# Kernel tuning notes

Hardware: AMD Instinct MI355X
Metric: run time of the kernel (lower is better)

The kernel has to match this reference:

```python
import jax, jax.numpy as jnp
import numpy as np

N = 50000      # nodes
F = 128        # in_features
OUT = 128      # out_features
E = 600000     # edges per adjacency (avg degree 12)
J = 2
BN_EPS = 1e-5


def setup_inputs() -> dict:
    key = jax.random.key(0)
    ks = jax.random.split(key, 10)
    x = jax.random.normal(ks[0], (N, F), dtype=jnp.float32)
    rows0 = jax.random.randint(ks[1], (E,), 0, N, dtype=jnp.int32)
    cols0 = jax.random.randint(ks[2], (E,), 0, N, dtype=jnp.int32)
    vals0 = jax.random.uniform(ks[3], (E,), dtype=jnp.float32)
    rows1 = jax.random.randint(ks[4], (E,), 0, N, dtype=jnp.int32)
    cols1 = jax.random.randint(ks[5], (E,), 0, N, dtype=jnp.int32)
    vals1 = jax.random.uniform(ks[6], (E,), dtype=jnp.float32)
    # Linear(J*F, OUT) params, torch default init U(-1/sqrt(fan_in), 1/sqrt(fan_in))
    lim = 1.0 / np.sqrt(J * F)
    W_fc = jax.random.uniform(ks[7], (OUT, J * F), dtype=jnp.float32, minval=-lim, maxval=lim)
    b_fc = jax.random.uniform(ks[8], (OUT,), dtype=jnp.float32, minval=-lim, maxval=lim)
    gamma = jnp.ones((OUT,), dtype=jnp.float32)
    beta = jnp.zeros((OUT,), dtype=jnp.float32)
    return {"x": x, "rows0": rows0, "cols0": cols0, "vals0": vals0,
            "rows1": rows1, "cols1": cols1, "vals1": vals1,
            "W_fc": W_fc, "b_fc": b_fc, "gamma": gamma, "beta": beta}


def _spmm(rows, cols, vals, x):
    # sparse [N,N] @ dense [N,F]: gather source features, weight, scatter-add to rows
    msgs = vals[:, None] * x[cols]                      # [E, F]
    return jax.ops.segment_sum(msgs, rows, num_segments=x.shape[0])  # [N, F]


def reference(x, rows0, cols0, vals0, rows1, cols1, vals1, W_fc, b_fc, gamma, beta):
    h = jnp.concatenate([_spmm(rows0, cols0, vals0, x),
                         _spmm(rows1, cols1, vals1, x)], axis=1)  # [N, J*F]
    y = h @ W_fc.T + b_fc                                         # [N, OUT]
    # BatchNorm1d (training mode: batch stats, biased variance)
    mean = jnp.mean(y, axis=0)
    var = jnp.mean((y - mean) ** 2, axis=0)
    return (y - mean) * jax.lax.rsqrt(var + BN_EPS) * gamma + beta
```

## Files before the change

### kernel.cpp

```cpp
#include <hip/hip_runtime.h>

#define N_NODES 50000
#define F_IN 128
#define OUT_F 128
#define JF 256
#define EDGES 600000
#define BN_EPS 1e-5f
#define MAXDEG 48
#define NPART 8
#define PART_ROWS 6250
#define BKCAP 163840
#define LCAP 256
#define EB_PER_SIDE 586
#define EDGE_B (2*EB_PER_SIDE)
#define CONVX_B 6250
#define CONVW_B 32
#define BUILDA_B (EDGE_B + CONVX_B + CONVW_B)
#define SCATB_B 1024
#define ROWS_PB 16
#define GATH_B 3125
#define GEMM_ROWS 32
#define GEMM_B 1563
#define HPAD 50048
#define NCOPY 16

typedef __attribute__((ext_vector_type(8))) short short8;
typedef __attribute__((ext_vector_type(4))) float floatx4;
typedef __attribute__((ext_vector_type(4))) unsigned short ushortx4;

static __device__ __forceinline__ unsigned short f2bf(float f) {
    unsigned int x = __float_as_uint(f);
    unsigned int r = (x + 0x7fffu + ((x >> 16) & 1u)) >> 16;
    return (unsigned short)r;
}
static __device__ __forceinline__ float bflo(unsigned int p) { return __uint_as_float(p << 16); }
static __device__ __forceinline__ float bfhi(unsigned int p) { return __uint_as_float(p & 0xffff0000u); }

__global__ __launch_bounds__(256) void build_a(
    const int* __restrict__ rows0, const int* __restrict__ cols0, const float* __restrict__ vals0,
    const int* __restrict__ rows1, const int* __restrict__ cols1, const float* __restrict__ vals1,
    uint2* __restrict__ buckets, int* __restrict__ gcur,
    const floatx4* __restrict__ x4, ushortx4* __restrict__ xb4,
    const float* __restrict__ W, uint2* __restrict__ Wb2)
{
    int bid = blockIdx.x;
    int tid = threadIdx.x;
    if (bid < EDGE_B) {
        __shared__ int   lcnt_[NPART];
        __shared__ int   lbase[NPART];
        __shared__ uint2 lbuf[NPART][LCAP];

        if (tid < NPART) lcnt_[tid] = 0;
        __syncthreads();

        int side = bid >= EB_PER_SIDE;
        int b = side ? bid - EB_PER_SIDE : bid;
        const int*   rows = side ? rows1 : rows0;
        const int*   cols = side ? cols1 : cols0;
        const float* vals = side ? vals1 : vals0;

        int e = b * 1024 + tid * 4;
        if (e < EDGES) {
            int4 rv = *(const int4*)(rows + e);
            int4 cv = *(const int4*)(cols + e);
            float4 vv = *(const float4*)(vals + e);
            int rr[4] = {rv.x, rv.y, rv.z, rv.w};
            int cc[4] = {cv.x, cv.y, cv.z, cv.w};
            float ff[4] = {vv.x, vv.y, vv.z, vv.w};
            #pragma unroll
            for (int j = 0; j < 4; ++j) {
                unsigned part = (unsigned)rr[j] / (unsigned)PART_ROWS;
                uint2 q;
                q.x = (unsigned)rr[j] | ((unsigned)side << 20);
                q.y = ((unsigned)cc[j] << 16) | f2bf(ff[j]);
                int pos = atomicAdd(&lcnt_[part], 1);
                if (pos < LCAP) {
                    lbuf[part][pos] = q;
                } else {
                    int gp = atomicAdd(&gcur[part], 1);
                    if (gp < BKCAP) buckets[(size_t)part * BKCAP + gp] = q;
                }
            }
        }
        __syncthreads();
        if (tid < NPART) {
            int c = lcnt_[tid]; if (c > LCAP) c = LCAP;
            lcnt_[tid] = c;
            lbase[tid] = atomicAdd(&gcur[tid], c);
        }
        __syncthreads();
        #pragma unroll
        for (int p = 0; p < NPART; ++p) {
            int c = lcnt_[p], base = lbase[p];
            for (int j = tid; j < c; j += 256) {
                int gp = base + j;
                if (gp < BKCAP) buckets[(size_t)p * BKCAP + gp] = lbuf[p][j];
            }
        }
    } else if (bid < EDGE_B + CONVX_B) {
        int i = (bid - EDGE_B) * 256 + tid;
        floatx4 v = __builtin_nontemporal_load(&x4[i]);
        ushortx4 o;
        o.x = f2bf(v.x); o.y = f2bf(v.y); o.z = f2bf(v.z); o.w = f2bf(v.w);
        __builtin_nontemporal_store(o, &xb4[i]);
    } else {
        int i = (bid - EDGE_B - CONVX_B) * 256 + tid;
        int col = i >> 6, l = i & 63;
        const float* wr = W + (size_t)col * JF;
        float a0 = wr[2 * l], a1 = wr[2 * l + 1];
        float b0 = wr[128 + 2 * l], b1 = wr[128 + 2 * l + 1];
        uint2 o;
        o.x = (unsigned int)f2bf(a0) | ((unsigned int)f2bf(a1) << 16);
        o.y = (unsigned int)f2bf(b0) | ((unsigned int)f2bf(b1) << 16);
        Wb2[col * 64 + l] = o;
    }
}

__global__ __launch_bounds__(256) void build_b(
    const uint2* __restrict__ buckets, const int* __restrict__ gcur,
    int* __restrict__ cnt0, int* __restrict__ cnt1,
    unsigned int* __restrict__ pe0, unsigned int* __restrict__ pe1)
{
    int part = blockIdx.x & (NPART - 1);
    int sub = blockIdx.x >> 3;
    int n = gcur[part]; if (n > BKCAP) n = BKCAP;
    const uint2* bk = buckets + (size_t)part * BKCAP;
    for (int i = sub * 256 + threadIdx.x; i < n; i += (SCATB_B / NPART) * 256) {
        uint2 q = bk[i];
        unsigned r = q.x & 0xFFFFFu;
        unsigned side = q.x >> 20;
        int* cnt = side ? cnt1 : cnt0;
        unsigned int* pe = side ? pe1 : pe0;
        int p = atomicAdd(&cnt[r], 1);
        if (p < MAXDEG) pe[(size_t)r * MAXDEG + p] = q.y;
    }
}

static __device__ __forceinline__ void rec_u(
    unsigned int q, int lane,
    const unsigned int* __restrict__ xb32, float& A0, float& A1)
{
    unsigned int xv = xb32[(q >> 16) * 64 + lane];
    float vv = __uint_as_float(q << 16);
    A0 += vv * bflo(xv);
    A1 += vv * bfhi(xv);
}
static __device__ __forceinline__ void rec_m(
    unsigned int q, bool on, int lane,
    const unsigned int* __restrict__ xb32, float& A0, float& A1)
{
    unsigned int idx = on ? (q >> 16) : 0u;
    float vv = on ? __uint_as_float(q << 16) : 0.0f;
    unsigned int xv = xb32[idx * 64 + lane];
    A0 += vv * bflo(xv);
    A1 += vv * bfhi(xv);
}

__global__ __launch_bounds__(256, 8) void gather_kernel(
    const unsigned int* __restrict__ xb32,
    const int* __restrict__ cnt0, const unsigned int* __restrict__ pe0,
    const int* __restrict__ cnt1, const unsigned int* __restrict__ pe1,
    uint2* __restrict__ hb)
{
    __shared__ uint4 recs[2][ROWS_PB][6];
    __shared__ int   lcnt[2][ROWS_PB];

    int tid = threadIdx.x;
    int lane = tid & 63;
    int w = tid >> 6;
    int wu = __builtin_amdgcn_readfirstlane(w);
    int row0 = blockIdx.x * ROWS_PB;

    if (tid < 192) {
        int lr = tid / 12;
        int rem = tid - lr * 12;
        int side = rem >= 6;
        int g = rem - side * 6;
        const unsigned int* pe = side ? pe1 : pe0;
        recs[side][lr][g] = *(const uint4*)(pe + (size_t)(row0 + lr) * MAXDEG + g * 4);
    }
    if (tid < 2 * ROWS_PB) {
        int side = tid >= ROWS_PB;
        int lr = tid & (ROWS_PB - 1);
        int d = (side ? cnt1 : cnt0)[row0 + lr];
        if (d > MAXDEG) d = MAXDEG;
        lcnt[side][lr] = d;
    }
    __syncthreads();

    for (int rr = 0; rr < 4; ++rr) {
        int lr = wu * 4 + rr;
        int r = row0 + lr;
        int d0 = __builtin_amdgcn_readfirstlane(lcnt[0][lr]);
        int d1 = __builtin_amdgcn_readfirstlane(lcnt[1][lr]);

        float aL0 = 0.f, aL1 = 0.f, aR0 = 0.f, aR1 = 0.f;

        #pragma unroll
        for (int g = 0; g < 6; ++g) {
            if (g * 4 < d0) {
                uint4 q = recs[0][lr][g];
                rec_u(q.x, lane, xb32, aL0, aL1);
                rec_m(q.y, g * 4 + 1 < d0, lane, xb32, aL0, aL1);
                rec_m(q.z, g * 4 + 2 < d0, lane, xb32, aL0, aL1);
                rec_m(q.w, g * 4 + 3 < d0, lane, xb32, aL0, aL1);
            }
        }
        #pragma unroll
        for (int g = 0; g < 6; ++g) {
            if (g * 4 < d1) {
                uint4 q = recs[1][lr][g];
                rec_u(q.x, lane, xb32, aR0, aR1);
                rec_m(q.y, g * 4 + 1 < d1, lane, xb32, aR0, aR1);
                rec_m(q.z, g * 4 + 2 < d1, lane, xb32, aR0, aR1);
                rec_m(q.w, g * 4 + 3 < d1, lane, xb32, aR0, aR1);
            }
        }
        if (d0 > 24)
            for (int p = 24; p < d0; ++p)
                rec_u(pe0[(size_t)r * MAXDEG + p], lane, xb32, aL0, aL1);
        if (d1 > 24)
            for (int p = 24; p < d1; ++p)
                rec_u(pe1[(size_t)r * MAXDEG + p], lane, xb32, aR0, aR1);

        uint2 o;
        o.x = (unsigned int)f2bf(aL0) | ((unsigned int)f2bf(aL1) << 16);
        o.y = (unsigned int)f2bf(aR0) | ((unsigned int)f2bf(aR1) << 16);
        hb[(size_t)r * 64 + lane] = o;
    }
}

__global__ __launch_bounds__(256, 6) void gemm_kernel(
    const char* __restrict__ hb,
    const ushort* __restrict__ Wb,
    const float* __restrict__ bias,
    float* __restrict__ y, float* __restrict__ stats)
{
    __shared__ float lstat[256];

    int tid = threadIdx.x;
    int lane = tid & 63;
    int w = tid >> 6;
    int row0 = blockIdx.x * GEMM_ROWS + (w & 1) * 16;
    int cbase = (w >> 1) * 64;

    lstat[tid] = 0.f;
    __syncthreads();

    int colb = lane & 15;
    int kg = lane >> 4;
    const char* abase = hb + (size_t)(row0 + colb) * 512 + kg * 16;

    floatx4 acc[4];
    #pragma unroll
    for (int c = 0; c < 4; ++c) acc[c] = (floatx4){0.f, 0.f, 0.f, 0.f};

    #pragma unroll
    for (int k0 = 0; k0 < 8; ++k0) {
        short8 a = *(const short8*)(abase + k0 * 64);
        #pragma unroll
        for (int c = 0; c < 4; ++c) {
            short8 b = *(const short8*)(Wb + (size_t)(cbase + c * 16 + colb) * 256 + k0 * 32 + kg * 8);
            acc[c] = __builtin_amdgcn_mfma_f32_16x16x32_bf16(a, b, acc[c], 0, 0, 0);
        }
    }

    #pragma unroll
    for (int c = 0; c < 4; ++c) {
        int col = cbase + c * 16 + colb;
        float bv = bias[col];
        float s = 0.f, s2 = 0.f;
        #pragma unroll
        for (int q = 0; q < 4; ++q) {
            int row = row0 + kg * 4 + q;
            if (row < N_NODES) {
                float val = acc[c][q] + bv;
                y[(size_t)row * OUT_F + col] = val;
                s += val; s2 += val * val;
            }
        }
        atomicAdd(&lstat[col], s);
        atomicAdd(&lstat[128 + col], s2);
    }
    __syncthreads();
    float* sdst = stats + (size_t)(blockIdx.x & (NCOPY - 1)) * 256;
    atomicAdd(&sdst[tid], lstat[tid]);
}

__global__ void bn_prep(const float* __restrict__ stats,
                        const float* __restrict__ gamma,
                        const float* __restrict__ beta,
                        float* __restrict__ ss)
{
    int o = threadIdx.x;
    if (o >= OUT_F) return;
    float s = 0.f, s2 = 0.f;
    #pragma unroll
    for (int c = 0; c < NCOPY; ++c) {
        s  += stats[c * 256 + o];
        s2 += stats[c * 256 + 128 + o];
    }
    float inv_n = 1.0f / (float)N_NODES;
    float mean = s * inv_n;
    float var  = s2 * inv_n - mean * mean;
    float sc = rsqrtf(var + BN_EPS) * gamma[o];
    ss[o] = sc;
    ss[OUT_F + o] = beta[o] - mean * sc;
}

__global__ __launch_bounds__(256) void bn_apply(
    float* __restrict__ y, const float* __restrict__ ss)
{
    size_t i = (size_t)blockIdx.x * blockDim.x + threadIdx.x;
    size_t total = (size_t)N_NODES * OUT_F / 4;
    if (i >= total) return;

    int c4 = (int)(i & (OUT_F / 4 - 1));
    float4 v  = ((const float4*)y)[i];
    float4 sc = ((const float4*)ss)[c4];
    float4 sh = ((const float4*)(ss + OUT_F))[c4];
    v.x = v.x * sc.x + sh.x;
    v.y = v.y * sc.y + sh.y;
    v.z = v.z * sc.z + sh.z;
    v.w = v.w * sc.w + sh.w;
    ((float4*)y)[i] = v;
}

extern "C" void kernel_launch(void* const* d_in, const int* in_sizes, int n_in,
                              void* d_out, int out_size, void* d_ws, size_t ws_size,
                              hipStream_t stream)
{
    const float* x     = (const float*)d_in[0];
    const int*   rows0 = (const int*)  d_in[1];
    const int*   cols0 = (const int*)  d_in[2];
    const float* vals0 = (const float*)d_in[3];
    const int*   rows1 = (const int*)  d_in[4];
    const int*   cols1 = (const int*)  d_in[5];
    const float* vals1 = (const float*)d_in[6];
    const float* W     = (const float*)d_in[7];
    const float* b     = (const float*)d_in[8];
    const float* gamma = (const float*)d_in[9];
    const float* beta  = (const float*)d_in[10];

    float* y = (float*)d_out;

    ushort* xb = (ushort*)d_ws;
    ushort* Wb = xb + (size_t)N_NODES * F_IN;
    unsigned int* pe0 = (unsigned int*)(Wb + OUT_F * JF);
    unsigned int* pe1 = pe0 + (size_t)N_NODES * MAXDEG;
    uint2* hb = (uint2*)(pe1 + (size_t)N_NODES * MAXDEG);
    uint2* buckets = hb;
    int* gcur = (int*)(hb + (size_t)HPAD * 64);
    int* cnt0 = gcur + NPART;
    int* cnt1 = cnt0 + N_NODES;
    float* stats = (float*)(cnt1 + N_NODES);
    float* ss    = stats + NCOPY * 256;

    hipMemsetAsync(gcur, 0,
                   ((size_t)NPART + 2 * N_NODES + NCOPY * 256) * sizeof(int),
                   stream);

    build_a<<<BUILDA_B, 256, 0, stream>>>(
        rows0, cols0, vals0, rows1, cols1, vals1,
        buckets, gcur,
        (const floatx4*)x, (ushortx4*)xb, W, (uint2*)Wb);

    build_b<<<SCATB_B, 256, 0, stream>>>(buckets, gcur, cnt0, cnt1, pe0, pe1);

    gather_kernel<<<GATH_B, 256, 0, stream>>>(
        (const unsigned int*)xb, cnt0, pe0, cnt1, pe1, hb);

    gemm_kernel<<<GEMM_B, 256, 0, stream>>>(
        (const char*)hb, Wb, b, y, stats);

    bn_prep<<<1, 128, 0, stream>>>(stats, gamma, beta, ss);
    bn_apply<<<CONVX_B, 256, 0, stream>>>(y, ss);
}
```

Baseline: 180.2 us.

## Use XCC-affine dynamic chunk scheduling with tickets in bucket scatter kernel

build_b now reads the hardware XCC id and has each block work first on the partition matching its XCC. Blocks claim 512-record chunks through per-partition atomic tickets and move on to other partitions once theirs is exhausted, with each thread handling two records through a 16-byte nontemporal load. The intent is to keep the atomics on each partition's row range local to one XCC's L2 and to balance the load dynamically. The cost is an extra atomic and two barriers per chunk, plus a dependence on partition-to-row locality lining up with XCC placement.

```diff
diff --git a/kernel.cpp b/kernel.cpp
--- a/kernel.cpp
+++ b/kernel.cpp
@@ -16,7 +16,8 @@
 #define CONVX_B 6250
 #define CONVW_B 32
 #define BUILDA_B (EDGE_B + CONVX_B + CONVW_B)
-#define SCATB_B 1024
+#define SCATB_B 2048
+#define CHUNK_REC 512
 #define ROWS_PB 16
 #define GATH_B 3125
 #define GEMM_ROWS 32
@@ -27,6 +28,7 @@
 typedef __attribute__((ext_vector_type(8))) short short8;
 typedef __attribute__((ext_vector_type(4))) float floatx4;
 typedef __attribute__((ext_vector_type(4))) unsigned short ushortx4;
+typedef __attribute__((ext_vector_type(4))) unsigned int uintx4;
 
 static __device__ __forceinline__ unsigned short f2bf(float f) {
     unsigned int x = __float_as_uint(f);
@@ -35,6 +37,12 @@
 }
 static __device__ __forceinline__ float bflo(unsigned int p) { return __uint_as_float(p << 16); }
 static __device__ __forceinline__ float bfhi(unsigned int p) { return __uint_as_float(p & 0xffff0000u); }
+
+static __device__ __forceinline__ unsigned xcc_id() {
+    unsigned x;
+    asm volatile("s_getreg_b32 %0, hwreg(HW_REG_XCC_ID, 0, 32)" : "=s"(x));
+    return x & (NPART - 1);
+}
 
 __global__ __launch_bounds__(256) void build_a(
     const int* __restrict__ rows0, const int* __restrict__ cols0, const float* __restrict__ vals0,
@@ -118,21 +126,48 @@
 
 __global__ __launch_bounds__(256) void build_b(
     const uint2* __restrict__ buckets, const int* __restrict__ gcur,
+    int* __restrict__ ticket,
     int* __restrict__ cnt0, int* __restrict__ cnt1,
     unsigned int* __restrict__ pe0, unsigned int* __restrict__ pe1)
 {
-    int part = blockIdx.x & (NPART - 1);
-    int sub = blockIdx.x >> 3;
-    int n = gcur[part]; if (n > BKCAP) n = BKCAP;
-    const uint2* bk = buckets + (size_t)part * BKCAP;
-    for (int i = sub * 256 + threadIdx.x; i < n; i += (SCATB_B / NPART) * 256) {
-        uint2 q = bk[i];
-        unsigned r = q.x & 0xFFFFFu;
-        unsigned side = q.x >> 20;
-        int* cnt = side ? cnt1 : cnt0;
-        unsigned int* pe = side ? pe1 : pe0;
-        int p = atomicAdd(&cnt[r], 1);
-        if (p < MAXDEG) pe[(size_t)r * MAXDEG + p] = q.y;
+    __shared__ int t_sh;
+    unsigned myp = xcc_id();
+    int tid = threadIdx.x;
+
+    for (int pp = 0; pp < NPART; ++pp) {
+        unsigned part = (myp + pp) & (NPART - 1);
+        int n = gcur[part]; if (n > BKCAP) n = BKCAP;
+        int nch = (n + CHUNK_REC - 1) / CHUNK_REC;
+        const uint2* bk = buckets + (size_t)part * BKCAP;
+
+        for (;;) {
+            __syncthreads();
+            if (tid == 0) t_sh = atomicAdd(&ticket[part], 1);
+            __syncthreads();
+            int t = t_sh;
+            if (t >= nch) break;
+
+            int base = t * CHUNK_REC + tid * 2;
+            if (base < n) {
+                uintx4 q2 = __builtin_nontemporal_load((const uintx4*)(bk + base));
+                {
+                    unsigned r = q2.x & 0xFFFFFu;
+                    unsigned side = q2.x >> 20;
+                    int* cnt = side ? cnt1 : cnt0;
+                    unsigned int* pe = side ? pe1 : pe0;
+                    int p = atomicAdd(&cnt[r], 1);
+                    if (p < MAXDEG) pe[(size_t)r * MAXDEG + p] = q2.y;
+                }
+                if (base + 1 < n) {
+                    unsigned r = q2.z & 0xFFFFFu;
+                    unsigned side = q2.z >> 20;
+                    int* cnt = side ? cnt1 : cnt0;
+                    unsigned int* pe = side ? pe1 : pe0;
+                    int p = atomicAdd(&cnt[r], 1);
+                    if (p < MAXDEG) pe[(size_t)r * MAXDEG + p] = q2.w;
+                }
+            }
+        }
     }
 }
 
@@ -351,13 +386,14 @@
     uint2* hb = (uint2*)(pe1 + (size_t)N_NODES * MAXDEG);
     uint2* buckets = hb;
     int* gcur = (int*)(hb + (size_t)HPAD * 64);
-    int* cnt0 = gcur + NPART;
+    int* ticket = gcur + NPART;
+    int* cnt0 = ticket + NPART;
     int* cnt1 = cnt0 + N_NODES;
     float* stats = (float*)(cnt1 + N_NODES);
     float* ss    = stats + NCOPY * 256;
 
     hipMemsetAsync(gcur, 0,
-                   ((size_t)NPART + 2 * N_NODES + NCOPY * 256) * sizeof(int),
+                   ((size_t)2 * NPART + 2 * N_NODES + NCOPY * 256) * sizeof(int),
                    stream);
 
     build_a<<<BUILDA_B, 256, 0, stream>>>(
@@ -365,7 +401,8 @@
         buckets, gcur,
         (const floatx4*)x, (ushortx4*)xb, W, (uint2*)Wb);
 
-    build_b<<<SCATB_B, 256, 0, stream>>>(buckets, gcur, cnt0, cnt1, pe0, pe1);
+    build_b<<<SCATB_B, 256, 0, stream>>>(buckets, gcur, ticket,
+                                         cnt0, cnt1, pe0, pe1);
 
     gather_kernel<<<GATH_B, 256, 0, stream>>>(
         (const unsigned int*)xb, cnt0, pe0, cnt1, pe1, hb);
```

New measurement: 372.3 us. +106.6%, slower.
